# Optimization experiments

Hardware: AMD Instinct MI355X
Metric: run time of the kernel (lower is better)

Reference implementation:

```python
import jax, jax.numpy as jnp
import numpy as np

B, Q, K, D = 8, 2048, 2048, 64

def setup_inputs() -> dict:
    key = jax.random.key(0)
    kq, kk, kv, kl = jax.random.split(key, 4)
    queries = jax.random.normal(kq, (B, Q, D), dtype=jnp.float32)
    keys = jax.random.normal(kk, (B, K, D), dtype=jnp.float32)
    values = jax.random.normal(kv, (B, K, D), dtype=jnp.float32)
    valid_lens = jax.random.randint(kl, (B,), 1, K + 1)  # at least 1 valid key
    return {"queries": queries, "keys": keys, "values": values, "valid_lens": valid_lens}

def reference(queries, keys, values, valid_lens):
    d = queries.shape[-1]
    # scores: [B, Q, K]
    scores = jnp.einsum("bqd,bkd->bqk", queries, keys) / jnp.sqrt(jnp.float32(d))
    # d2l-style masked softmax: positions >= valid_len get -1e6 before softmax
    kpos = jnp.arange(scores.shape[-1])  # [K]
    mask = kpos[None, None, :] < valid_lens[:, None, None]  # [B,1,K]
    scores = jnp.where(mask, scores, jnp.float32(-1e6))
    attn = jax.nn.softmax(scores, axis=-1)
    # dropout is identity at inference (training=False)
    return jnp.einsum("bqk,bkd->bqd", attn, values)
```

## Files before the change

### kernel.cpp

```cpp
#include <hip/hip_runtime.h>

typedef float    f32x4  __attribute__((ext_vector_type(4)));
typedef float    f32x16 __attribute__((ext_vector_type(16)));
typedef _Float16 half8  __attribute__((ext_vector_type(8)));

constexpr int NB = 8;
constexpr int NQ = 2048;
constexpr int NKEY = 2048;
constexpr int DD = 64;
constexpr int KB = 64;

#define QSCALE (0.125f * 1.44269504088896340736f)

__device__ inline unsigned pkh(float a, float b) {
    return __builtin_bit_cast(unsigned, __builtin_amdgcn_cvt_pkrtz(a, b));
}
__device__ inline int vswz(int d) {
    return (((d >> 3) & 3) | ((d & 1) << 2)) << 4;
}

__device__ __forceinline__ void pv_chunk(
    const f32x16& sv, const char* __restrict__ vsm, int koff,
    int hi, int ql, int swzq, f32x16& o0, f32x16& o1)
{
    const unsigned w0 = pkh(sv[0],  sv[1]),  w1 = pkh(sv[2],  sv[3]);
    const unsigned w2 = pkh(sv[4],  sv[5]),  w3 = pkh(sv[6],  sv[7]);
    const unsigned w4 = pkh(sv[8],  sv[9]),  w5 = pkh(sv[10], sv[11]);
    const unsigned w6 = pkh(sv[12], sv[13]), w7 = pkh(sv[14], sv[15]);
    const unsigned p0 = __shfl_xor(w0, 32), p1 = __shfl_xor(w1, 32);
    const unsigned p2 = __shfl_xor(w2, 32), p3 = __shfl_xor(w3, 32);
    const unsigned p4 = __shfl_xor(w4, 32), p5 = __shfl_xor(w5, 32);
    const unsigned p6 = __shfl_xor(w6, 32), p7 = __shfl_xor(w7, 32);
    const bool h1 = (hi != 0);
    union { unsigned u[4]; half8 h; } A0, A1;
    A0.u[0] = h1 ? p2 : w0;  A0.u[1] = h1 ? p3 : w1;
    A0.u[2] = h1 ? w2 : p0;  A0.u[3] = h1 ? w3 : p1;
    A1.u[0] = h1 ? p6 : w4;  A1.u[1] = h1 ? p7 : w5;
    A1.u[2] = h1 ? w6 : p4;  A1.u[3] = h1 ? w7 : p5;

    __builtin_amdgcn_s_setprio(1);
#pragma unroll
    for (int t = 0; t < 2; ++t) {
        const int co = koff + t * 32 + hi * 16;
        const half8 vb0 = *(const half8*)(vsm + ql * 128        + (co ^ swzq));
        const half8 vb1 = *(const half8*)(vsm + (32 + ql) * 128 + (co ^ swzq));
        const half8 pa = (t == 0) ? A0.h : A1.h;
        o0 = __builtin_amdgcn_mfma_f32_32x32x16_f16(pa, vb0, o0, 0, 0, 0);
        o1 = __builtin_amdgcn_mfma_f32_32x32x16_f16(pa, vb1, o1, 0, 0, 0);
    }
    __builtin_amdgcn_s_setprio(0);
}

__global__ __launch_bounds__(256, 2) void attn_fused(
    const float* __restrict__ Qp, const float* __restrict__ Kp,
    const float* __restrict__ Vp, const int* __restrict__ VL,
    float* __restrict__ Op)
{
    __shared__ __align__(16) char pool[65536];

    const int tid  = threadIdx.x;
    const int wv   = tid >> 6;
    const int lane = tid & 63;
    const int ql   = lane & 31;
    const int hi   = lane >> 5;

    char* Ksm = pool + wv * 16384;
    char* Vsm = Ksm + 8192;

    const int g  = blockIdx.x;
    const int b  = (g >> 3) & 7;
    const int qt = ((g >> 6) << 3) | (g & 7);
    const int qbase = qt * 32;

    const int vlen = VL[b];
    const int numt = (vlen + KB - 1) / KB;

    const float* qsrc = Qp + ((size_t)b * NQ + qbase + ql) * DD;
    half8 qf[4];
#pragma unroll
    for (int c = 0; c < 4; ++c) {
        f32x4 f0 = *(const f32x4*)(qsrc + c * 16 + hi * 8);
        f32x4 f1 = *(const f32x4*)(qsrc + c * 16 + hi * 8 + 4);
        half8 h;
#pragma unroll
        for (int j = 0; j < 4; ++j) {
            h[j]     = (_Float16)(f0[j] * QSCALE);
            h[4 + j] = (_Float16)(f1[j] * QSCALE);
        }
        qf[c] = h;
    }

    f32x16 o0 = {}, o1 = {};
    float mrun = -1e30f, lrun = 0.f;

    const int kr_ = lane >> 3;
    const int kd0 = (lane & 7) * 8;
    const int vk2 = (lane >> 4) * 2;
    const int vd0 = (lane & 15) * 4;
    const int swzq = vswz(ql);

    for (int t = wv; t < numt; t += 4) {
        const int kbase = t * KB;
        const float* kbp = Kp + ((size_t)b * NKEY + kbase) * DD;
        const float* vbp = Vp + ((size_t)b * NKEY + kbase) * DD;

        f32x4 ka[8][2];
#pragma unroll
        for (int i = 0; i < 8; ++i) {
            const float* src = kbp + (size_t)(i * 8 + kr_) * DD + kd0;
            ka[i][0] = *(const f32x4*)src;
            ka[i][1] = *(const f32x4*)(src + 4);
        }
        f32x4 va[8][2];
#pragma unroll
        for (int i = 0; i < 8; ++i) {
            const float* src = vbp + (size_t)(i * 8 + vk2) * DD + vd0;
            va[i][0] = *(const f32x4*)src;
            va[i][1] = *(const f32x4*)(src + DD);
        }

#pragma unroll
        for (int i = 0; i < 8; ++i) {
            half8 h;
#pragma unroll
            for (int j = 0; j < 4; ++j) {
                h[j]     = (_Float16)ka[i][0][j];
                h[4 + j] = (_Float16)ka[i][1][j];
            }
            const int off = ((i * 8 + kr_) * 128 + kd0 * 2) ^ (kr_ << 4);
            *(half8*)(Ksm + off) = h;
        }

        f32x16 svA = {}, svB = {};
        __builtin_amdgcn_s_setprio(1);
#pragma unroll
        for (int c = 0; c < 4; ++c) {
            const half8 kfA = *(const half8*)(Ksm +
                ((ql * 128 + c * 32 + hi * 16) ^ ((ql & 7) << 4)));
            svA = __builtin_amdgcn_mfma_f32_32x32x16_f16(kfA, qf[c], svA, 0, 0, 0);
            const half8 kfB = *(const half8*)(Ksm +
                (((32 + ql) * 128 + c * 32 + hi * 16) ^ ((ql & 7) << 4)));
            svB = __builtin_amdgcn_mfma_f32_32x32x16_f16(kfB, qf[c], svB, 0, 0, 0);
        }
        __builtin_amdgcn_s_setprio(0);

#pragma unroll
        for (int i = 0; i < 8; ++i) {
#pragma unroll
            for (int jj = 0; jj < 4; ++jj) {
                const int d = vd0 + jj;
                const unsigned w = pkh(va[i][0][jj], va[i][1][jj]);
                *(unsigned*)(Vsm + d * 128 + (((i * 16 + vk2 * 2)) ^ vswz(d))) = w;
            }
        }

        if (kbase + KB > vlen) {
#pragma unroll
            for (int r = 0; r < 16; ++r) {
                const int krow = (r & 3) + 8 * (r >> 2) + 4 * hi;
                svA[r] = (kbase + krow < vlen)      ? svA[r] : -1e30f;
                svB[r] = (kbase + 32 + krow < vlen) ? svB[r] : -1e30f;
            }
        }

        float mx[16];
#pragma unroll
        for (int r = 0; r < 16; ++r) mx[r] = fmaxf(svA[r], svB[r]);
#pragma unroll
        for (int st = 8; st > 0; st >>= 1)
#pragma unroll
            for (int r = 0; r < st; ++r) mx[r] = fmaxf(mx[r], mx[r + st]);
        float mr = fmaxf(mx[0], __shfl_xor(mx[0], 32));

        if (!__all(mr <= mrun + 8.f)) {
            const float mn = fmaxf(mrun, mr);
            const float alpha = __builtin_amdgcn_exp2f(mrun - mn);
            lrun *= alpha;
            mrun = mn;
#pragma unroll
            for (int r = 0; r < 16; ++r) {
                const int qr = (r & 3) + 8 * (r >> 2) + 4 * hi;
                const float ar = __shfl(alpha, qr);
                o0[r] *= ar;
                o1[r] *= ar;
            }
        }

#pragma unroll
        for (int r = 0; r < 16; ++r) {
            svA[r] = __builtin_amdgcn_exp2f(svA[r] - mrun);
            svB[r] = __builtin_amdgcn_exp2f(svB[r] - mrun);
        }
        float sx[16];
#pragma unroll
        for (int r = 0; r < 16; ++r) sx[r] = svA[r] + svB[r];
#pragma unroll
        for (int st = 8; st > 0; st >>= 1)
#pragma unroll
            for (int r = 0; r < st; ++r) sx[r] += sx[r + st];
        lrun += sx[0] + __shfl_xor(sx[0], 32);

        pv_chunk(svA, Vsm, 0,  hi, ql, swzq, o0, o1);
        pv_chunk(svB, Vsm, 64, hi, ql, swzq, o0, o1);
    }

    __syncthreads();
    float* Mb = (float*)(pool + 32768);
    float* Lb = (float*)(pool + 32768 + 512);
    float* Tb = (float*)(pool + 32768 + 1024);
    float (*Obuf)[32][64] = (float (*)[32][64])pool;

    if (hi == 0) { Mb[wv * 32 + ql] = mrun; Lb[wv * 32 + ql] = lrun; }
    __syncthreads();

    float Mtot = -1e30f;
#pragma unroll
    for (int w = 0; w < 4; ++w)
        if (Lb[w * 32 + ql] > 0.f) Mtot = fmaxf(Mtot, Mb[w * 32 + ql]);
    float Ltot = 0.f;
#pragma unroll
    for (int w = 0; w < 4; ++w) {
        const float lw = Lb[w * 32 + ql];
        if (lw > 0.f) Ltot += lw * __builtin_amdgcn_exp2f(Mb[w * 32 + ql] - Mtot);
    }
    const float wown = (lrun > 0.f) ? __builtin_amdgcn_exp2f(mrun - Mtot) : 0.f;
    if (wv == 0 && hi == 0) Tb[ql] = Ltot;

#pragma unroll
    for (int r = 0; r < 16; ++r) {
        const int qr = (r & 3) + 8 * (r >> 2) + 4 * hi;
        const float wr = __shfl(wown, qr);
        Obuf[wv][qr][ql]      = o0[r] * wr;
        Obuf[wv][qr][ql + 32] = o1[r] * wr;
    }
    __syncthreads();

#pragma unroll
    for (int k = 0; k < 8; ++k) {
        const int q = wv * 8 + k;
        const float sum = Obuf[0][q][lane] + Obuf[1][q][lane]
                        + Obuf[2][q][lane] + Obuf[3][q][lane];
        Op[((size_t)b * NQ + qbase + q) * DD + lane] = sum / Tb[q];
    }
}

extern "C" void kernel_launch(void* const* d_in, const int* in_sizes, int n_in,
                              void* d_out, int out_size, void* d_ws, size_t ws_size,
                              hipStream_t stream) {
    const float* Qp = (const float*)d_in[0];
    const float* Kp = (const float*)d_in[1];
    const float* Vp = (const float*)d_in[2];
    const int*   VL = (const int*)d_in[3];
    float* Op = (float*)d_out;

    dim3 block(256);
    dim3 grid(NB * (NQ / 32));
    hipLaunchKernelGGL(attn_fused, grid, block, 0, stream, Qp, Kp, Vp, VL, Op);
}
```

Baseline: 31.04 us.

## Split key range across eight waves with 32-key tiles per wave

Each workgroup now runs 8 waves (512 threads) and each wave handles 32-key tiles instead of 64-key ones. This doubles the parallel split of the key dimension per query tile, and the LDS layout and swizzle are reworked for the smaller K/V tiles. The block-to-(batch, query tile) mapping is changed, and the final cross-wave reduction is vectorised over 8 partial outputs. The aim is more latency hiding and better balance on short valid lengths, at the cost of more merge work, more shared memory per block, and fewer blocks resident per CU.

```diff
diff --git a/kernel.cpp b/kernel.cpp
--- a/kernel.cpp
+++ b/kernel.cpp
@@ -8,19 +8,16 @@
 constexpr int NQ = 2048;
 constexpr int NKEY = 2048;
 constexpr int DD = 64;
-constexpr int KB = 64;
+constexpr int KB = 32;
 
 #define QSCALE (0.125f * 1.44269504088896340736f)
 
 __device__ inline unsigned pkh(float a, float b) {
     return __builtin_bit_cast(unsigned, __builtin_amdgcn_cvt_pkrtz(a, b));
 }
-__device__ inline int vswz(int d) {
-    return (((d >> 3) & 3) | ((d & 1) << 2)) << 4;
-}
 
 __device__ __forceinline__ void pv_chunk(
-    const f32x16& sv, const char* __restrict__ vsm, int koff,
+    const f32x16& sv, const char* __restrict__ vsm,
     int hi, int ql, int swzq, f32x16& o0, f32x16& o1)
 {
     const unsigned w0 = pkh(sv[0],  sv[1]),  w1 = pkh(sv[2],  sv[3]);
@@ -41,9 +38,9 @@
     __builtin_amdgcn_s_setprio(1);
 #pragma unroll
     for (int t = 0; t < 2; ++t) {
-        const int co = koff + t * 32 + hi * 16;
-        const half8 vb0 = *(const half8*)(vsm + ql * 128        + (co ^ swzq));
-        const half8 vb1 = *(const half8*)(vsm + (32 + ql) * 128 + (co ^ swzq));
+        const int co = t * 32 + hi * 16;
+        const half8 vb0 = *(const half8*)(vsm + ql * 64        + (co ^ swzq));
+        const half8 vb1 = *(const half8*)(vsm + (32 + ql) * 64 + (co ^ swzq));
         const half8 pa = (t == 0) ? A0.h : A1.h;
         o0 = __builtin_amdgcn_mfma_f32_32x32x16_f16(pa, vb0, o0, 0, 0, 0);
         o1 = __builtin_amdgcn_mfma_f32_32x32x16_f16(pa, vb1, o1, 0, 0, 0);
@@ -51,12 +48,12 @@
     __builtin_amdgcn_s_setprio(0);
 }
 
-__global__ __launch_bounds__(256, 2) void attn_fused(
+__global__ __launch_bounds__(512, 4) void attn_fused(
     const float* __restrict__ Qp, const float* __restrict__ Kp,
     const float* __restrict__ Vp, const int* __restrict__ VL,
     float* __restrict__ Op)
 {
-    __shared__ __align__(16) char pool[65536];
+    __shared__ __align__(16) char pool[67584];
 
     const int tid  = threadIdx.x;
     const int wv   = tid >> 6;
@@ -64,12 +61,12 @@
     const int ql   = lane & 31;
     const int hi   = lane >> 5;
 
-    char* Ksm = pool + wv * 16384;
-    char* Vsm = Ksm + 8192;
+    char* Ksm = pool + wv * 8192;
+    char* Vsm = Ksm + 4096;
 
     const int g  = blockIdx.x;
-    const int b  = (g >> 3) & 7;
-    const int qt = ((g >> 6) << 3) | (g & 7);
+    const int b  = ((g >> 3) & 7) ^ ((g >> 8) << 2);
+    const int qt = (g & 7) | (((g >> 6) & 7) << 3);
     const int qbase = qt * 32;
 
     const int vlen = VL[b];
@@ -97,60 +94,58 @@
     const int kd0 = (lane & 7) * 8;
     const int vk2 = (lane >> 4) * 2;
     const int vd0 = (lane & 15) * 4;
-    const int swzq = vswz(ql);
-
-    for (int t = wv; t < numt; t += 4) {
+    const int swzq = (ql & 3) << 4;
+
+    for (int t = wv; t < numt; t += 8) {
         const int kbase = t * KB;
         const float* kbp = Kp + ((size_t)b * NKEY + kbase) * DD;
         const float* vbp = Vp + ((size_t)b * NKEY + kbase) * DD;
 
-        f32x4 ka[8][2];
-#pragma unroll
-        for (int i = 0; i < 8; ++i) {
+        f32x4 ka[4][2];
+#pragma unroll
+        for (int i = 0; i < 4; ++i) {
             const float* src = kbp + (size_t)(i * 8 + kr_) * DD + kd0;
             ka[i][0] = *(const f32x4*)src;
             ka[i][1] = *(const f32x4*)(src + 4);
         }
-        f32x4 va[8][2];
-#pragma unroll
-        for (int i = 0; i < 8; ++i) {
+#pragma unroll
+        for (int i = 0; i < 4; ++i) {
+            half8 h;
+#pragma unroll
+            for (int j = 0; j < 4; ++j) {
+                h[j]     = (_Float16)ka[i][0][j];
+                h[4 + j] = (_Float16)ka[i][1][j];
+            }
+            const int off = ((i * 8 + kr_) * 128 + kd0 * 2) ^ (kr_ << 4);
+            *(half8*)(Ksm + off) = h;
+        }
+
+        f32x4 va[4][2];
+#pragma unroll
+        for (int i = 0; i < 4; ++i) {
             const float* src = vbp + (size_t)(i * 8 + vk2) * DD + vd0;
             va[i][0] = *(const f32x4*)src;
             va[i][1] = *(const f32x4*)(src + DD);
         }
 
-#pragma unroll
-        for (int i = 0; i < 8; ++i) {
-            half8 h;
-#pragma unroll
-            for (int j = 0; j < 4; ++j) {
-                h[j]     = (_Float16)ka[i][0][j];
-                h[4 + j] = (_Float16)ka[i][1][j];
-            }
-            const int off = ((i * 8 + kr_) * 128 + kd0 * 2) ^ (kr_ << 4);
-            *(half8*)(Ksm + off) = h;
-        }
-
-        f32x16 svA = {}, svB = {};
+        f32x16 sv = {};
         __builtin_amdgcn_s_setprio(1);
 #pragma unroll
         for (int c = 0; c < 4; ++c) {
-            const half8 kfA = *(const half8*)(Ksm +
+            const half8 kf = *(const half8*)(Ksm +
                 ((ql * 128 + c * 32 + hi * 16) ^ ((ql & 7) << 4)));
-            svA = __builtin_amdgcn_mfma_f32_32x32x16_f16(kfA, qf[c], svA, 0, 0, 0);
-            const half8 kfB = *(const half8*)(Ksm +
-                (((32 + ql) * 128 + c * 32 + hi * 16) ^ ((ql & 7) << 4)));
-            svB = __builtin_amdgcn_mfma_f32_32x32x16_f16(kfB, qf[c], svB, 0, 0, 0);
+            sv = __builtin_amdgcn_mfma_f32_32x32x16_f16(kf, qf[c], sv, 0, 0, 0);
         }
         __builtin_amdgcn_s_setprio(0);
 
 #pragma unroll
-        for (int i = 0; i < 8; ++i) {
+        for (int i = 0; i < 4; ++i) {
 #pragma unroll
             for (int jj = 0; jj < 4; ++jj) {
                 const int d = vd0 + jj;
+                const int k = i * 4 + (lane >> 4);
                 const unsigned w = pkh(va[i][0][jj], va[i][1][jj]);
-                *(unsigned*)(Vsm + d * 128 + (((i * 16 + vk2 * 2)) ^ vswz(d))) = w;
+                *(unsigned*)(Vsm + d * 64 + ((k * 4) ^ ((d & 3) << 4))) = w;
             }
         }
 
@@ -158,14 +153,13 @@
 #pragma unroll
             for (int r = 0; r < 16; ++r) {
                 const int krow = (r & 3) + 8 * (r >> 2) + 4 * hi;
-                svA[r] = (kbase + krow < vlen)      ? svA[r] : -1e30f;
-                svB[r] = (kbase + 32 + krow < vlen) ? svB[r] : -1e30f;
+                sv[r] = (kbase + krow < vlen) ? sv[r] : -1e30f;
             }
         }
 
         float mx[16];
 #pragma unroll
-        for (int r = 0; r < 16; ++r) mx[r] = fmaxf(svA[r], svB[r]);
+        for (int r = 0; r < 16; ++r) mx[r] = sv[r];
 #pragma unroll
         for (int st = 8; st > 0; st >>= 1)
 #pragma unroll
@@ -187,27 +181,23 @@
         }
 
 #pragma unroll
-        for (int r = 0; r < 16; ++r) {
-            svA[r] = __builtin_amdgcn_exp2f(svA[r] - mrun);
-            svB[r] = __builtin_amdgcn_exp2f(svB[r] - mrun);
-        }
+        for (int r = 0; r < 16; ++r)
+            sv[r] = __builtin_amdgcn_exp2f(sv[r] - mrun);
         float sx[16];
 #pragma unroll
-        for (int r = 0; r < 16; ++r) sx[r] = svA[r] + svB[r];
+        for (int r = 0; r < 16; ++r) sx[r] = sv[r];
 #pragma unroll
         for (int st = 8; st > 0; st >>= 1)
 #pragma unroll
             for (int r = 0; r < st; ++r) sx[r] += sx[r + st];
         lrun += sx[0] + __shfl_xor(sx[0], 32);
 
-        pv_chunk(svA, Vsm, 0,  hi, ql, swzq, o0, o1);
-        pv_chunk(svB, Vsm, 64, hi, ql, swzq, o0, o1);
+        pv_chunk(sv, Vsm, hi, ql, swzq, o0, o1);
     }
 
     __syncthreads();
-    float* Mb = (float*)(pool + 32768);
-    float* Lb = (float*)(pool + 32768 + 512);
-    float* Tb = (float*)(pool + 32768 + 1024);
+    float* Mb = (float*)(pool + 65536);
+    float* Lb = (float*)(pool + 65536 + 1024);
     float (*Obuf)[32][64] = (float (*)[32][64])pool;
 
     if (hi == 0) { Mb[wv * 32 + ql] = mrun; Lb[wv * 32 + ql] = lrun; }
@@ -215,16 +205,9 @@
 
     float Mtot = -1e30f;
 #pragma unroll
-    for (int w = 0; w < 4; ++w)
+    for (int w = 0; w < 8; ++w)
         if (Lb[w * 32 + ql] > 0.f) Mtot = fmaxf(Mtot, Mb[w * 32 + ql]);
-    float Ltot = 0.f;
-#pragma unroll
-    for (int w = 0; w < 4; ++w) {
-        const float lw = Lb[w * 32 + ql];
-        if (lw > 0.f) Ltot += lw * __builtin_amdgcn_exp2f(Mb[w * 32 + ql] - Mtot);
-    }
     const float wown = (lrun > 0.f) ? __builtin_amdgcn_exp2f(mrun - Mtot) : 0.f;
-    if (wv == 0 && hi == 0) Tb[ql] = Ltot;
 
 #pragma unroll
     for (int r = 0; r < 16; ++r) {
@@ -235,12 +218,28 @@
     }
     __syncthreads();
 
-#pragma unroll
-    for (int k = 0; k < 8; ++k) {
-        const int q = wv * 8 + k;
-        const float sum = Obuf[0][q][lane] + Obuf[1][q][lane]
-                        + Obuf[2][q][lane] + Obuf[3][q][lane];
-        Op[((size_t)b * NQ + qbase + q) * DD + lane] = sum / Tb[q];
+    {
+        const int q  = tid >> 4;
+        const int d0 = (tid & 15) * 4;
+        float Mq = -1e30f;
+#pragma unroll
+        for (int w = 0; w < 8; ++w)
+            if (Lb[w * 32 + q] > 0.f) Mq = fmaxf(Mq, Mb[w * 32 + q]);
+        float Ltot = 0.f;
+#pragma unroll
+        for (int w = 0; w < 8; ++w) {
+            const float lw = Lb[w * 32 + q];
+            if (lw > 0.f) Ltot += lw * __builtin_amdgcn_exp2f(Mb[w * 32 + q] - Mq);
+        }
+        f32x4 acc = {};
+#pragma unroll
+        for (int w = 0; w < 8; ++w)
+            acc += *(const f32x4*)(&Obuf[w][q][d0]);
+        const float inv = 1.0f / Ltot;
+        f32x4 outv;
+#pragma unroll
+        for (int j = 0; j < 4; ++j) outv[j] = acc[j] * inv;
+        *(f32x4*)(Op + ((size_t)b * NQ + qbase + q) * DD + d0) = outv;
     }
 }
 
@@ -253,7 +252,7 @@
     const int*   VL = (const int*)d_in[3];
     float* Op = (float*)d_out;
 
-    dim3 block(256);
+    dim3 block(512);
     dim3 grid(NB * (NQ / 32));
     hipLaunchKernelGGL(attn_fused, grid, block, 0, stream, Qp, Kp, Vp, VL, Op);
 }
```

After: 45.84 us. +47.7%, slower.

## Pre-convert K/V to swizzled fp16 tiles and stream them via global_load_lds

Applied to the files above, without the earlier changes.

Adds a pre-pass kernel that converts K to fp16 and V to a transposed fp16 layout, both written as pre-swizzled 64-key tiles in the workspace. The attention kernel then copies each tile straight into LDS with global_load_lds and waits on vmcnt, instead of loading fp32, converting and scattering per block. It also remaps block indices so different batches interleave. This removes the repeated fp32 loads and per-block conversion work, at the cost of a second launch and an extra round trip of K/V through memory.

```diff
diff --git a/kernel.cpp b/kernel.cpp
--- a/kernel.cpp
+++ b/kernel.cpp
@@ -9,6 +9,8 @@
 constexpr int NKEY = 2048;
 constexpr int DD = 64;
 constexpr int KB = 64;
+constexpr int NT = NKEY / KB;
+constexpr size_t TILE_BYTES = (size_t)KB * DD * 2;
 
 #define QSCALE (0.125f * 1.44269504088896340736f)
 
@@ -17,6 +19,62 @@
 }
 __device__ inline int vswz(int d) {
     return (((d >> 3) & 3) | ((d & 1) << 2)) << 4;
+}
+
+#define GLL(gp, lp) __builtin_amdgcn_global_load_lds( \
+    (const __attribute__((address_space(1))) void*)(gp), \
+    (__attribute__((address_space(3))) void*)(lp), 16, 0, 0)
+
+__global__ __launch_bounds__(256) void convert_kv(
+    const float* __restrict__ Kp, const float* __restrict__ Vp,
+    char* __restrict__ Kh, char* __restrict__ Vt)
+{
+    __shared__ __align__(16) char vbuf[64 * 144];
+    const int g    = blockIdx.x;
+    const bool isV = (g >= NB * NT);
+    const int bt   = isV ? g - NB * NT : g;
+    const int tid  = threadIdx.x;
+    const int k    = tid >> 2;
+    const int c    = tid & 3;
+
+    const int b = bt >> 5, T = bt & 31;
+    const float* src = (isV ? Vp : Kp) + ((size_t)b * NKEY + T * 64 + k) * DD + c * 16;
+    half8 lo, hi;
+#pragma unroll
+    for (int j = 0; j < 2; ++j) {
+        f32x4 f0 = *(const f32x4*)(src + j * 8);
+        f32x4 f1 = *(const f32x4*)(src + j * 8 + 4);
+#pragma unroll
+        for (int i = 0; i < 4; ++i) {
+            if (j == 0) { lo[i] = (_Float16)f0[i]; lo[4 + i] = (_Float16)f1[i]; }
+            else        { hi[i] = (_Float16)f0[i]; hi[4 + i] = (_Float16)f1[i]; }
+        }
+    }
+
+    if (!isV) {
+        char* dst = Kh + (size_t)bt * TILE_BYTES;
+        const int base = k * 128 + c * 32;
+        const int swz  = (k & 7) << 4;
+        *(half8*)(dst + (base ^ swz))        = lo;
+        *(half8*)(dst + ((base + 16) ^ swz)) = hi;
+    } else {
+        *(half8*)(vbuf + k * 144 + c * 32)      = lo;
+        *(half8*)(vbuf + k * 144 + c * 32 + 16) = hi;
+        __syncthreads();
+        const int d  = tid >> 2;
+        const int c2 = tid & 3;
+        half8 l2, h2;
+#pragma unroll
+        for (int j = 0; j < 8; ++j) {
+            l2[j] = *(const _Float16*)(vbuf + (c2 * 16 + j) * 144 + d * 2);
+            h2[j] = *(const _Float16*)(vbuf + (c2 * 16 + 8 + j) * 144 + d * 2);
+        }
+        char* dst = Vt + (size_t)bt * TILE_BYTES;
+        const int base = d * 128 + c2 * 32;
+        const int swz  = vswz(d);
+        *(half8*)(dst + (base ^ swz))        = l2;
+        *(half8*)(dst + ((base + 16) ^ swz)) = h2;
+    }
 }
 
 __device__ __forceinline__ void pv_chunk(
@@ -52,8 +110,8 @@
 }
 
 __global__ __launch_bounds__(256, 2) void attn_fused(
-    const float* __restrict__ Qp, const float* __restrict__ Kp,
-    const float* __restrict__ Vp, const int* __restrict__ VL,
+    const float* __restrict__ Qp, const char* __restrict__ Kh,
+    const char* __restrict__ Vt, const int* __restrict__ VL,
     float* __restrict__ Op)
 {
     __shared__ __align__(16) char pool[65536];
@@ -68,8 +126,9 @@
     char* Vsm = Ksm + 8192;
 
     const int g  = blockIdx.x;
-    const int b  = (g >> 3) & 7;
-    const int qt = ((g >> 6) << 3) | (g & 7);
+    const int m  = g >> 3;
+    const int b  = (m ^ (m >> 3)) & 7;
+    const int qt = (g & 7) | ((m >> 3) << 3);
     const int qbase = qt * 32;
 
     const int vlen = VL[b];
@@ -92,44 +151,20 @@
 
     f32x16 o0 = {}, o1 = {};
     float mrun = -1e30f, lrun = 0.f;
-
-    const int kr_ = lane >> 3;
-    const int kd0 = (lane & 7) * 8;
-    const int vk2 = (lane >> 4) * 2;
-    const int vd0 = (lane & 15) * 4;
     const int swzq = vswz(ql);
 
     for (int t = wv; t < numt; t += 4) {
         const int kbase = t * KB;
-        const float* kbp = Kp + ((size_t)b * NKEY + kbase) * DD;
-        const float* vbp = Vp + ((size_t)b * NKEY + kbase) * DD;
-
-        f32x4 ka[8][2];
-#pragma unroll
-        for (int i = 0; i < 8; ++i) {
-            const float* src = kbp + (size_t)(i * 8 + kr_) * DD + kd0;
-            ka[i][0] = *(const f32x4*)src;
-            ka[i][1] = *(const f32x4*)(src + 4);
-        }
-        f32x4 va[8][2];
-#pragma unroll
-        for (int i = 0; i < 8; ++i) {
-            const float* src = vbp + (size_t)(i * 8 + vk2) * DD + vd0;
-            va[i][0] = *(const f32x4*)src;
-            va[i][1] = *(const f32x4*)(src + DD);
-        }
-
-#pragma unroll
-        for (int i = 0; i < 8; ++i) {
-            half8 h;
-#pragma unroll
-            for (int j = 0; j < 4; ++j) {
-                h[j]     = (_Float16)ka[i][0][j];
-                h[4 + j] = (_Float16)ka[i][1][j];
-            }
-            const int off = ((i * 8 + kr_) * 128 + kd0 * 2) ^ (kr_ << 4);
-            *(half8*)(Ksm + off) = h;
-        }
+        const char* ksrc = Kh + (size_t)(b * NT + t) * TILE_BYTES + lane * 16;
+        const char* vsrc = Vt + (size_t)(b * NT + t) * TILE_BYTES + lane * 16;
+
+        __builtin_amdgcn_sched_barrier(0);
+#pragma unroll
+        for (int j = 0; j < 8; ++j) GLL(ksrc + j * 1024, Ksm + j * 1024);
+#pragma unroll
+        for (int j = 0; j < 8; ++j) GLL(vsrc + j * 1024, Vsm + j * 1024);
+        asm volatile("s_waitcnt vmcnt(8)" ::: "memory");
+        __builtin_amdgcn_sched_barrier(0);
 
         f32x16 svA = {}, svB = {};
         __builtin_amdgcn_s_setprio(1);
@@ -144,16 +179,6 @@
         }
         __builtin_amdgcn_s_setprio(0);
 
-#pragma unroll
-        for (int i = 0; i < 8; ++i) {
-#pragma unroll
-            for (int jj = 0; jj < 4; ++jj) {
-                const int d = vd0 + jj;
-                const unsigned w = pkh(va[i][0][jj], va[i][1][jj]);
-                *(unsigned*)(Vsm + d * 128 + (((i * 16 + vk2 * 2)) ^ vswz(d))) = w;
-            }
-        }
-
         if (kbase + KB > vlen) {
 #pragma unroll
             for (int r = 0; r < 16; ++r) {
@@ -200,6 +225,8 @@
             for (int r = 0; r < st; ++r) sx[r] += sx[r + st];
         lrun += sx[0] + __shfl_xor(sx[0], 32);
 
+        asm volatile("s_waitcnt vmcnt(0)" ::: "memory");
+        __builtin_amdgcn_sched_barrier(0);
         pv_chunk(svA, Vsm, 0,  hi, ql, swzq, o0, o1);
         pv_chunk(svB, Vsm, 64, hi, ql, swzq, o0, o1);
     }
@@ -253,7 +280,12 @@
     const int*   VL = (const int*)d_in[3];
     float* Op = (float*)d_out;
 
+    char* Kh = (char*)d_ws;
+    char* Vt = (char*)d_ws + (size_t)NB * NT * TILE_BYTES;
+
     dim3 block(256);
-    dim3 grid(NB * (NQ / 32));
-    hipLaunchKernelGGL(attn_fused, grid, block, 0, stream, Qp, Kp, Vp, VL, Op);
-}
+    hipLaunchKernelGGL(convert_kv, dim3(2 * NB * NT), block, 0, stream,
+                       Kp, Vp, Kh, Vt);
+    hipLaunchKernelGGL(attn_fused, dim3(NB * (NQ / 32)), block, 0, stream,
+                       Qp, Kh, Vt, VL, Op);
+}
```

Measured after the change: 30.81 us. Within noise of the previous version (-0.8%).
